# Performance work log

Hardware: AMD Instinct MI355X
Metric: run time of the kernel (lower is better)

Reference implementation:

```python
import jax, jax.numpy as jnp
import numpy as np

N_NODES = 100000
N_EDGES = 1000000
VOCAB = 128
EMB = 64
HID = 64
N_CLASSES = 2
N_GRAPHS = 2048


def setup_inputs() -> dict:
    key = jax.random.key(0)
    ks = jax.random.split(key, 12)
    x = jax.random.randint(ks[0], (N_NODES,), 0, VOCAB)
    edge_index = jax.random.randint(ks[1], (2, N_EDGES), 0, N_NODES)
    batch = jnp.sort(jax.random.randint(ks[2], (N_NODES,), 0, N_GRAPHS))

    def glorot(k, shape):
        fan = shape[0]
        return jax.random.normal(k, shape, dtype=jnp.float32) / np.sqrt(fan).astype(np.float32)

    emb = jax.random.normal(ks[3], (VOCAB, EMB), dtype=jnp.float32)
    W1_l = glorot(ks[4], (EMB, HID)); b1 = jnp.zeros((HID,), jnp.float32)
    W1_r = glorot(ks[5], (EMB, HID))
    W2_l = glorot(ks[6], (HID, HID)); b2 = jnp.zeros((HID,), jnp.float32)
    W2_r = glorot(ks[7], (HID, HID))
    W_out = glorot(ks[8], (HID, N_CLASSES)); b_out = jnp.zeros((N_CLASSES,), jnp.float32)
    return {"x": x, "edge_index": edge_index, "batch": batch, "emb": emb,
            "W1_l": W1_l, "b1": b1, "W1_r": W1_r,
            "W2_l": W2_l, "b2": b2, "W2_r": W2_r,
            "W_out": W_out, "b_out": b_out}


def _sage_conv(h, src, dst, Wl, bl, Wr):
    # PyG SAGEConv: out = lin_l(mean_{j in N(i)} h_j) + lin_r(h_i); lin_r has no bias
    msgs = h[src]                                                        # [E, D] gather
    agg = jax.ops.segment_sum(msgs, dst, num_segments=N_NODES)          # [N, D] scatter-add
    cnt = jax.ops.segment_sum(jnp.ones((src.shape[0], 1), h.dtype), dst,
                              num_segments=N_NODES)                      # [N, 1] degree
    mean = agg / jnp.maximum(cnt, 1.0)
    return mean @ Wl + bl + h @ Wr


def reference(x, edge_index, batch, emb, W1_l, b1, W1_r, W2_l, b2, W2_r, W_out, b_out):
    src, dst = edge_index[0], edge_index[1]
    h = emb[x]                                                           # [N, EMB]
    h = jax.nn.relu(_sage_conv(h, src, dst, W1_l, b1, W1_r))             # [N, HID]
    h = jax.nn.relu(_sage_conv(h, src, dst, W2_l, b2, W2_r))             # [N, HID]
    # global_mean_pool over graph ids
    gsum = jax.ops.segment_sum(h, batch, num_segments=N_GRAPHS)          # [G, HID]
    gcnt = jax.ops.segment_sum(jnp.ones((N_NODES, 1), h.dtype), batch,
                               num_segments=N_GRAPHS)
    pooled = gsum / jnp.maximum(gcnt, 1.0)
    return pooled @ W_out + b_out                                        # [G, C]
```

## Files before the change

kernel.cpp:

```cpp
#include <hip/hip_runtime.h>
#include <hip/hip_bf16.h>

#define N_NODES 100000
#define N_EDGES 1000000
#define EMB 64
#define HID 64
#define VOCAB 128
#define N_GRAPHS 2048

#define CBUCKET 256
#define NBK ((N_NODES + CBUCKET - 1) / CBUCKET)
#define CAP 4096
#define CHUNK 4096
#define SCAT_BLOCKS ((N_EDGES + CHUNK - 1) / CHUNK)
#define GB ((N_NODES + 255) / 256)
#define ZROW N_NODES

#define BCASTF(v, l) __int_as_float(__builtin_amdgcn_readlane(__float_as_int(v), (l)))

typedef __attribute__((ext_vector_type(8))) short short8;
typedef __attribute__((ext_vector_type(4))) float f32x4;
typedef __attribute__((ext_vector_type(2))) float f32x2;

__device__ __forceinline__ float bf2f(unsigned short u) {
    return __uint_as_float((unsigned)u << 16);
}
__device__ __forceinline__ float bf2f_lo(unsigned u) {
    return __uint_as_float(u << 16);
}
__device__ __forceinline__ float bf2f_hi(unsigned u) {
    return __uint_as_float(u & 0xffff0000u);
}
__device__ __forceinline__ unsigned short f2bf(float f) {
    return __bfloat16_as_ushort(__float2bfloat16(f));
}

__global__ __launch_bounds__(256) void scatter_kernel(
    const int* __restrict__ src, const int* __restrict__ dst,
    const int* __restrict__ x,
    int* __restrict__ cursor, unsigned* __restrict__ edge8,
    const int* __restrict__ batch, int* __restrict__ gstart,
    const float* __restrict__ emb, const float* __restrict__ W1l,
    const float* __restrict__ W1r,
    const float* __restrict__ W2l, const float* __restrict__ W2r,
    float* __restrict__ embW1l, float* __restrict__ embW1r,
    unsigned short* __restrict__ w2frag, unsigned char* __restrict__ p8z)
{
    __shared__ unsigned earr[CHUNK];
    __shared__ unsigned short karr[CHUNK];
    __shared__ int bcnt[NBK];
    __shared__ int bbase[NBK];
    int b = blockIdx.x;
    int t = threadIdx.x;

    if (b < SCAT_BLOCKS) {
        for (int i = t; i < NBK; i += 256) bcnt[i] = 0;
        __syncthreads();
        int e0 = b * CHUNK;
        int n = min(e0 + CHUNK, N_EDGES) - e0;
        for (int i = t; i < n; i += 256) {
            int d = dst[e0 + i];
            int s = src[e0 + i];
            int xv = x[s];
            int k = d >> 8;
            earr[i] = (unsigned)s | ((unsigned)xv << 17) | ((unsigned)(d & 255) << 24);
            karr[i] = (unsigned short)k;
            atomicAdd(&bcnt[k], 1);
        }
        __syncthreads();
        for (int i = t; i < NBK; i += 256) {
            int c = bcnt[i];
            bbase[i] = i * CAP + (c ? atomicAdd(&cursor[i], c) : 0);
            bcnt[i] = 0;
        }
        __syncthreads();
        for (int i = t; i < n; i += 256) {
            int k = karr[i];
            int off = atomicAdd(&bcnt[k], 1);
            edge8[bbase[k] + off] = earr[i];
        }
    } else if (b < SCAT_BLOCKS + GB) {
        int i = (b - SCAT_BLOCKS) * 256 + t;
        if (i >= N_NODES) return;
        int bg = batch[i];
        int bp = (i == 0) ? -1 : batch[i - 1];
        for (int g = bp + 1; g <= bg; ++g) gstart[g] = i;
        if (i == N_NODES - 1)
            for (int g = bg + 1; g <= N_GRAPHS; ++g) gstart[g] = N_NODES;
    } else {
        int vb = b - SCAT_BLOCKS - GB;
        if (vb == 0 && t < 16)
            ((unsigned*)(p8z + (size_t)N_NODES * 64))[t] = 0u;
        int wave = t >> 6, lane = t & 63;
        int v = vb * 4 + wave;
        if (v < VOCAB) {
            float er = emb[v * 64 + lane];
            float al = 0.f, ar = 0.f;
#pragma unroll 8
            for (int d = 0; d < 64; ++d) {
                float e = BCASTF(er, d);
                al += e * W1l[d * 64 + lane];
                ar += e * W1r[d * 64 + lane];
            }
            embW1l[v * 64 + lane] = al;
            embW1r[v * 64 + lane] = ar;
        }
        int g = vb * 256 + t;
        int j = g & 7, l = (g >> 3) & 63, h = (g >> 9) & 1, tt = g >> 10;
        int k = h * 32 + ((l >> 4) * 8) + j;
        int n = tt * 16 + (l & 15);
        float w = (n < 64) ? W2l[k * 64 + n] : W2r[k * 64 + (n - 64)];
        w2frag[g] = f2bf(w);
    }
}

__global__ __launch_bounds__(256) void csr_kernel(
    const unsigned* __restrict__ edge8, const int* __restrict__ cursor,
    int* __restrict__ row_start, int* __restrict__ deg, int* __restrict__ col,
    int* __restrict__ col16,
    const float* __restrict__ embW1l, const float* __restrict__ embW1r,
    unsigned short* __restrict__ w1frag)
{
    __shared__ int cnt[CBUCKET];
    __shared__ int scn[CBUCKET];
    __shared__ int exs[CBUCKET];
    int b = blockIdx.x;
    int t = threadIdx.x;

    for (int i = t * 4; i < CBUCKET * 16; i += 1024)
        *(int4*)&col16[b * CBUCKET * 16 + i] = (int4){ZROW, ZROW, ZROW, ZROW};

    if (b < 8) {
        int g0 = (b * 256 + t) * 8;
#pragma unroll
        for (int j = 0; j < 8; ++j) {
            int g = g0 + j;
            int fi = g >> 9;
            int kf = fi >> 2, nt = fi & 3;
            int l = (g >> 3) & 63, jj = g & 7;
            int kg = kf * 32 + ((l >> 4) << 3) + jj;
            int n = nt * 16 + (l & 15);
            float w = (kg < 128) ? embW1l[kg * 64 + n] : embW1r[(kg - 128) * 64 + n];
            w1frag[g] = f2bf(w);
        }
    }

    int lo = b * CAP, hi = lo + cursor[b];
    cnt[t] = 0;
    __syncthreads();
    for (int i = lo + t; i < hi; i += 256)
        atomicAdd(&cnt[edge8[i] >> 24], 1);
    __syncthreads();
    int v = cnt[t];
    scn[t] = v;
    __syncthreads();
    for (int off = 1; off < 256; off <<= 1) {
        int tmp = (t >= off) ? scn[t - off] : 0;
        __syncthreads();
        scn[t] += tmp;
        __syncthreads();
    }
    int excl = scn[t] - v;
    int node = b * CBUCKET + t;
    if (node < N_NODES) { row_start[node] = lo + excl; deg[node] = v; }
    cnt[t] = excl;
    exs[t] = excl;
    __syncthreads();
    for (int i = lo + t; i < hi; i += 256) {
        unsigned e = edge8[i];
        int ld = (int)(e >> 24);
        int slot = atomicAdd(&cnt[ld], 1);
        col[lo + slot] = (int)(e & 0xFFFFFF);
        int local = slot - exs[ld];
        if (local < 16)
            col16[(b * CBUCKET + ld) * 16 + local] = (int)(e & 0x1FFFF);
    }
}

__global__ __launch_bounds__(256) void sage1_kernel(
    const int* __restrict__ x, const int* __restrict__ deg,
    const unsigned* __restrict__ edge8, const int* __restrict__ cursor,
    const unsigned short* __restrict__ w1frag,
    const unsigned short* __restrict__ w2frag, const float* __restrict__ b1,
    unsigned char* __restrict__ p8, unsigned short* __restrict__ q16)
{
    __shared__ unsigned hist[128 * 32];
    __shared__ unsigned short msbuf[128 * 72];
    __shared__ int xl[128];
    __shared__ float invd[128];

    int blk = blockIdx.x, bucket = blk >> 1, half = blk & 1;
    int t = threadIdx.x;
    int nbase = bucket * CBUCKET + half * 128;

    for (int i = t * 4; i < 128 * 32; i += 1024)
        *(uint4*)&hist[i] = (uint4){0u, 0u, 0u, 0u};
    if (t < 128) {
        int node = nbase + t;
        int dv = (node < N_NODES) ? deg[node] : 0;
        invd[t] = 1.0f / fmaxf((float)dv, 1.0f);
        xl[t] = (node < N_NODES) ? x[node] : 0;
    }
    __syncthreads();

    int lo = bucket * CAP, ecnt = cursor[bucket];
    for (int i = t; i < ecnt; i += 256) {
        unsigned e = edge8[lo + i];
        int ld = (int)(e >> 24);
        if ((ld >> 7) == half) {
            int r = ld & 127;
            int xv = (int)((e >> 17) & 127);
            int wc = (xv >> 2) ^ ((r & 7) << 2);
            atomicAdd(&hist[r * 32 + wc], 1u << ((xv & 3) * 8));
        }
    }
    __syncthreads();

    int wave = t >> 6, lane = t & 63;
    int m = lane & 15;
    int qd = lane >> 4;
    int hswz = (m & 7) << 2;

#pragma unroll
    for (int rt = wave * 2; rt < wave * 2 + 2; ++rt) {
        short8 acnt[4], aself[4];
#pragma unroll
        for (int kf = 0; kf < 4; ++kf) {
            int w0 = (kf * 8 + qd * 2) ^ hswz;
            uint2 u = *(const uint2*)&hist[(rt * 16 + m) * 32 + w0];
            short8 f;
            f[0] = (short)f2bf((float)(u.x & 255));
            f[1] = (short)f2bf((float)((u.x >> 8) & 255));
            f[2] = (short)f2bf((float)((u.x >> 16) & 255));
            f[3] = (short)f2bf((float)(u.x >> 24));
            f[4] = (short)f2bf((float)(u.y & 255));
            f[5] = (short)f2bf((float)((u.y >> 8) & 255));
            f[6] = (short)f2bf((float)((u.y >> 16) & 255));
            f[7] = (short)f2bf((float)(u.y >> 24));
            acnt[kf] = f;
        }
        int xv = xl[rt * 16 + m];
#pragma unroll
        for (int kf = 0; kf < 4; ++kf) {
            int v = xv - kf * 32 - qd * 8;
            short8 f;
#pragma unroll
            for (int j = 0; j < 8; ++j)
                f[j] = (v == j) ? (short)0x3F80 : (short)0;
            aself[kf] = f;
        }
        float iv0 = invd[rt * 16 + qd * 4 + 0];
        float iv1 = invd[rt * 16 + qd * 4 + 1];
        float iv2 = invd[rt * 16 + qd * 4 + 2];
        float iv3 = invd[rt * 16 + qd * 4 + 3];

#pragma unroll
        for (int nt = 0; nt < 4; ++nt) {
            f32x4 accA = {0.f, 0.f, 0.f, 0.f};
            f32x4 accS = {0.f, 0.f, 0.f, 0.f};
#pragma unroll
            for (int kf = 0; kf < 4; ++kf) {
                short8 bA = *(const short8*)(w1frag + ((kf * 4 + nt) * 64 + lane) * 8);
                accA = __builtin_amdgcn_mfma_f32_16x16x32_bf16(acnt[kf], bA, accA, 0, 0, 0);
            }
#pragma unroll
            for (int kf = 0; kf < 4; ++kf) {
                short8 bS = *(const short8*)(w1frag + (((kf + 4) * 4 + nt) * 64 + lane) * 8);
                accS = __builtin_amdgcn_mfma_f32_16x16x32_bf16(aself[kf], bS, accS, 0, 0, 0);
            }
            int c = nt * 16 + m;
            float b1c = b1[c];
            int rb = rt * 16 + qd * 4;
            msbuf[(rb + 0) * 72 + c] = f2bf(fmaxf(accA[0] * iv0 + accS[0] + b1c, 0.f));
            msbuf[(rb + 1) * 72 + c] = f2bf(fmaxf(accA[1] * iv1 + accS[1] + b1c, 0.f));
            msbuf[(rb + 2) * 72 + c] = f2bf(fmaxf(accA[2] * iv2 + accS[2] + b1c, 0.f));
            msbuf[(rb + 3) * 72 + c] = f2bf(fmaxf(accA[3] * iv3 + accS[3] + b1c, 0.f));
        }
    }
    __syncthreads();

#pragma unroll
    for (int rt = wave * 2; rt < wave * 2 + 2; ++rt) {
        const unsigned short* arow = &msbuf[(rt * 16 + m) * 72 + qd * 8];
        short8 a0 = *(const short8*)(arow);
        short8 a1 = *(const short8*)(arow + 32);
        int rowb = nbase + rt * 16 + qd * 4;

#pragma unroll
        for (int tt = 0; tt < 8; ++tt) {
            short8 b0 = *(const short8*)(w2frag + tt * 1024 + lane * 8);
            short8 b1v = *(const short8*)(w2frag + tt * 1024 + 512 + lane * 8);
            f32x4 acc = {0.f, 0.f, 0.f, 0.f};
            acc = __builtin_amdgcn_mfma_f32_16x16x32_bf16(a0, b0, acc, 0, 0, 0);
            acc = __builtin_amdgcn_mfma_f32_16x16x32_bf16(a1, b1v, acc, 0, 0, 0);
            int o = tt * 16 + m;
            if (o < 64) {
                int pk01 = __builtin_amdgcn_cvt_pk_fp8_f32(acc[0], acc[1], 0, false);
                int pk23 = __builtin_amdgcn_cvt_pk_fp8_f32(acc[2], acc[3], 0, false);
                if (rowb + 0 < N_NODES) p8[(rowb + 0) * 64 + o] = (unsigned char)(pk01 & 0xff);
                if (rowb + 1 < N_NODES) p8[(rowb + 1) * 64 + o] = (unsigned char)((pk01 >> 8) & 0xff);
                if (rowb + 2 < N_NODES) p8[(rowb + 2) * 64 + o] = (unsigned char)(pk23 & 0xff);
                if (rowb + 3 < N_NODES) p8[(rowb + 3) * 64 + o] = (unsigned char)((pk23 >> 8) & 0xff);
            } else {
                int oc = o & 63;
#pragma unroll
                for (int i = 0; i < 4; ++i)
                    if (rowb + i < N_NODES)
                        q16[(rowb + i) * 64 + oc] = f2bf(acc[i]);
            }
        }
    }
}

#define S2_NPW 8
__global__ __launch_bounds__(256) void sage2_kernel(
    const unsigned char* __restrict__ p, const unsigned short* __restrict__ q,
    const int* __restrict__ row_start, const int* __restrict__ deg,
    const int* __restrict__ col, const int* __restrict__ col16,
    const float* __restrict__ b2,
    const float* __restrict__ Wout, const int* __restrict__ batch,
    float* __restrict__ gsum)
{
    int t = threadIdx.x;
    int wave = t >> 6, lane = t & 63;
    int base_node = (blockIdx.x * 4 + wave) * S2_NPW;
    int c = lane & 15;
    int g = lane >> 4;

    float4 b2v = ((const float4*)b2)[c];
    float4 w01 = ((const float4*)Wout)[c * 2];
    float4 w23 = ((const float4*)Wout)[c * 2 + 1];

    int dgs[S2_NPW];
#pragma unroll
    for (int n = 0; n < S2_NPW; ++n)
        dgs[n] = deg[base_node + n];

#define ACC(a, v) { f32x2 f01_ = __builtin_amdgcn_cvt_pk_f32_fp8((int)(v), false); \
                    f32x2 f23_ = __builtin_amdgcn_cvt_pk_f32_fp8((int)(v), true);  \
                    (a).x += f01_.x; (a).y += f01_.y; (a).z += f23_.x; (a).w += f23_.y; }

#pragma unroll
    for (int hb = 0; hb < 2; ++hb) {
        int nb = hb * 4;

        unsigned vc = (unsigned)((base_node + nb) * 64 + g * 4);
        unsigned i00, i01, i02, i03, i10, i11, i12, i13;
        unsigned i20, i21, i22, i23, i30, i31, i32, i33;
        asm volatile(
            "global_load_dword %0,  %16, %17\n\t"
            "global_load_dword %1,  %16, %17 offset:16\n\t"
            "global_load_dword %2,  %16, %17 offset:32\n\t"
            "global_load_dword %3,  %16, %17 offset:48\n\t"
            "global_load_dword %4,  %16, %17 offset:64\n\t"
            "global_load_dword %5,  %16, %17 offset:80\n\t"
            "global_load_dword %6,  %16, %17 offset:96\n\t"
            "global_load_dword %7,  %16, %17 offset:112\n\t"
            "global_load_dword %8,  %16, %17 offset:128\n\t"
            "global_load_dword %9,  %16, %17 offset:144\n\t"
            "global_load_dword %10, %16, %17 offset:160\n\t"
            "global_load_dword %11, %16, %17 offset:176\n\t"
            "global_load_dword %12, %16, %17 offset:192\n\t"
            "global_load_dword %13, %16, %17 offset:208\n\t"
            "global_load_dword %14, %16, %17 offset:224\n\t"
            "global_load_dword %15, %16, %17 offset:240\n\t"
            "s_waitcnt vmcnt(0)"
            : "=&v"(i00), "=&v"(i01), "=&v"(i02), "=&v"(i03),
              "=&v"(i10), "=&v"(i11), "=&v"(i12), "=&v"(i13),
              "=&v"(i20), "=&v"(i21), "=&v"(i22), "=&v"(i23),
              "=&v"(i30), "=&v"(i31), "=&v"(i32), "=&v"(i33)
            : "v"(vc), "s"(col16)
            : "memory");

        unsigned cc4 = (unsigned)(c << 2);
        unsigned o00 = (i00 << 6) + cc4, o01 = (i01 << 6) + cc4;
        unsigned o02 = (i02 << 6) + cc4, o03 = (i03 << 6) + cc4;
        unsigned o10 = (i10 << 6) + cc4, o11 = (i11 << 6) + cc4;
        unsigned o12 = (i12 << 6) + cc4, o13 = (i13 << 6) + cc4;
        unsigned o20 = (i20 << 6) + cc4, o21 = (i21 << 6) + cc4;
        unsigned o22 = (i22 << 6) + cc4, o23 = (i23 << 6) + cc4;
        unsigned o30 = (i30 << 6) + cc4, o31 = (i31 << 6) + cc4;
        unsigned o32 = (i32 << 6) + cc4, o33 = (i33 << 6) + cc4;
        unsigned vq = (unsigned)((base_node + nb) * 128 + c * 8);

        unsigned v00, v01, v02, v03, v10, v11, v12, v13;
        unsigned v20, v21, v22, v23, v30, v31, v32, v33;
        unsigned qa0, qb0, qa1, qb1, qa2, qb2, qa3, qb3;
        asm volatile(
            "global_load_dword %0,  %24, %41\n\t"
            "global_load_dword %1,  %25, %41\n\t"
            "global_load_dword %2,  %26, %41\n\t"
            "global_load_dword %3,  %27, %41\n\t"
            "global_load_dword %4,  %28, %41\n\t"
            "global_load_dword %5,  %29, %41\n\t"
            "global_load_dword %6,  %30, %41\n\t"
            "global_load_dword %7,  %31, %41\n\t"
            "global_load_dword %8,  %32, %41\n\t"
            "global_load_dword %9,  %33, %41\n\t"
            "global_load_dword %10, %34, %41\n\t"
            "global_load_dword %11, %35, %41\n\t"
            "global_load_dword %12, %36, %41\n\t"
            "global_load_dword %13, %37, %41\n\t"
            "global_load_dword %14, %38, %41\n\t"
            "global_load_dword %15, %39, %41\n\t"
            "global_load_dword %16, %40, %42\n\t"
            "global_load_dword %17, %40, %42 offset:4\n\t"
            "global_load_dword %18, %40, %42 offset:128\n\t"
            "global_load_dword %19, %40, %42 offset:132\n\t"
            "global_load_dword %20, %40, %42 offset:256\n\t"
            "global_load_dword %21, %40, %42 offset:260\n\t"
            "global_load_dword %22, %40, %42 offset:384\n\t"
            "global_load_dword %23, %40, %42 offset:388\n\t"
            "s_waitcnt vmcnt(0)"
            : "=&v"(v00), "=&v"(v01), "=&v"(v02), "=&v"(v03),
              "=&v"(v10), "=&v"(v11), "=&v"(v12), "=&v"(v13),
              "=&v"(v20), "=&v"(v21), "=&v"(v22), "=&v"(v23),
              "=&v"(v30), "=&v"(v31), "=&v"(v32), "=&v"(v33),
              "=&v"(qa0), "=&v"(qb0), "=&v"(qa1), "=&v"(qb1),
              "=&v"(qa2), "=&v"(qb2), "=&v"(qa3), "=&v"(qb3)
            : "v"(o00), "v"(o01), "v"(o02), "v"(o03),
              "v"(o10), "v"(o11), "v"(o12), "v"(o13),
              "v"(o20), "v"(o21), "v"(o22), "v"(o23),
              "v"(o30), "v"(o31), "v"(o32), "v"(o33),
              "v"(vq), "s"(p), "s"(q)
            : "memory");

#pragma unroll
        for (int pp = 0; pp < 2; ++pp) {
            int na = nb + pp * 2, nbd = nb + pp * 2 + 1;
            int dgA = dgs[na], dgB = dgs[nbd];

            float4 aA = {0.f,0.f,0.f,0.f}, aB = {0.f,0.f,0.f,0.f};
            if (pp == 0) {
                ACC(aA, v00) ACC(aA, v01) ACC(aA, v02) ACC(aA, v03)
                ACC(aB, v10) ACC(aB, v11) ACC(aB, v12) ACC(aB, v13)
            } else {
                ACC(aA, v20) ACC(aA, v21) ACC(aA, v22) ACC(aA, v23)
                ACC(aB, v30) ACC(aB, v31) ACC(aB, v32) ACC(aB, v33)
            }

            if (dgA > 16) {
                int rsA = row_start[base_node + na];
                for (int j = 16; j < dgA; j += 8) {
                    int r0 = j + g, r1 = j + 4 + g;
                    int i0 = (r0 < dgA) ? (col[rsA + r0] & 0x1FFFF) : ZROW;
                    int i1 = (r1 < dgA) ? (col[rsA + r1] & 0x1FFFF) : ZROW;
                    unsigned u0 = *(const unsigned*)(p + (size_t)i0 * 64 + c * 4);
                    unsigned u1 = *(const unsigned*)(p + (size_t)i1 * 64 + c * 4);
                    ACC(aA, u0) ACC(aA, u1)
                }
            }
            if (dgB > 16) {
                int rsB = row_start[base_node + nbd];
                for (int j = 16; j < dgB; j += 8) {
                    int r0 = j + g, r1 = j + 4 + g;
                    int i0 = (r0 < dgB) ? (col[rsB + r0] & 0x1FFFF) : ZROW;
                    int i1 = (r1 < dgB) ? (col[rsB + r1] & 0x1FFFF) : ZROW;
                    unsigned u0 = *(const unsigned*)(p + (size_t)i0 * 64 + c * 4);
                    unsigned u1 = *(const unsigned*)(p + (size_t)i1 * 64 + c * 4);
                    ACC(aB, u0) ACC(aB, u1)
                }
            }

            aA.x += __shfl_xor(aA.x, 16, 64); aA.y += __shfl_xor(aA.y, 16, 64);
            aA.z += __shfl_xor(aA.z, 16, 64); aA.w += __shfl_xor(aA.w, 16, 64);
            aB.x += __shfl_xor(aB.x, 16, 64); aB.y += __shfl_xor(aB.y, 16, 64);
            aB.z += __shfl_xor(aB.z, 16, 64); aB.w += __shfl_xor(aB.w, 16, 64);
            aA.x += __shfl_xor(aA.x, 32, 64); aA.y += __shfl_xor(aA.y, 32, 64);
            aA.z += __shfl_xor(aA.z, 32, 64); aA.w += __shfl_xor(aA.w, 32, 64);
            aB.x += __shfl_xor(aB.x, 32, 64); aB.y += __shfl_xor(aB.y, 32, 64);
            aB.z += __shfl_xor(aB.z, 32, 64); aB.w += __shfl_xor(aB.w, 32, 64);

#pragma unroll
            for (int e = 0; e < 2; ++e) {
                int node = base_node + nb + pp * 2 + e;
                int dg = (e == 0) ? dgA : dgB;
                float4 a = (e == 0) ? aA : aB;
                int li = pp * 2 + e;
                unsigned qlo = (li == 0) ? qa0 : (li == 1) ? qa1 : (li == 2) ? qa2 : qa3;
                unsigned qhi = (li == 0) ? qb0 : (li == 1) ? qb1 : (li == 2) ? qb2 : qb3;
                float inv = 1.0f / fmaxf((float)dg, 1.0f);
                float h0 = fmaxf(a.x * inv + b2v.x + bf2f_lo(qlo), 0.f);
                float h1 = fmaxf(a.y * inv + b2v.y + bf2f_hi(qlo), 0.f);
                float h2 = fmaxf(a.z * inv + b2v.z + bf2f_lo(qhi), 0.f);
                float h3 = fmaxf(a.w * inv + b2v.w + bf2f_hi(qhi), 0.f);

                float p0 = h0 * w01.x + h1 * w01.z + h2 * w23.x + h3 * w23.z;
                float p1 = h0 * w01.y + h1 * w01.w + h2 * w23.y + h3 * w23.w;
                if (g != 0) { p0 = 0.f; p1 = 0.f; }
                p0 += __shfl_down(p0, 8, 64);  p1 += __shfl_down(p1, 8, 64);
                p0 += __shfl_down(p0, 4, 64);  p1 += __shfl_down(p1, 4, 64);
                p0 += __shfl_down(p0, 2, 64);  p1 += __shfl_down(p1, 2, 64);
                p0 += __shfl_down(p0, 1, 64);  p1 += __shfl_down(p1, 1, 64);
                if (lane == 0) {
                    int grp = batch[node];
                    atomicAdd(&gsum[grp * 2 + 0], p0);
                    atomicAdd(&gsum[grp * 2 + 1], p1);
                }
            }
        }
    }
#undef ACC
}

__global__ __launch_bounds__(256) void finalize_kernel(
    const float* __restrict__ gsum, const int* __restrict__ gstart,
    const float* __restrict__ bout, float* __restrict__ out)
{
    int g = blockIdx.x * 256 + threadIdx.x;
    if (g >= N_GRAPHS) return;
    int cnt = gstart[g + 1] - gstart[g];
    float inv = 1.0f / fmaxf((float)cnt, 1.0f);
    out[g * 2 + 0] = gsum[g * 2 + 0] * inv + bout[0];
    out[g * 2 + 1] = gsum[g * 2 + 1] * inv + bout[1];
}

extern "C" void kernel_launch(void* const* d_in, const int* in_sizes, int n_in,
                              void* d_out, int out_size, void* d_ws, size_t ws_size,
                              hipStream_t stream) {
    const int*   x    = (const int*)  d_in[0];
    const int*   ei   = (const int*)  d_in[1];
    const int*   batch= (const int*)  d_in[2];
    const float* emb  = (const float*)d_in[3];
    const float* W1l  = (const float*)d_in[4];
    const float* b1   = (const float*)d_in[5];
    const float* W1r  = (const float*)d_in[6];
    const float* W2l  = (const float*)d_in[7];
    const float* b2   = (const float*)d_in[8];
    const float* W2r  = (const float*)d_in[9];
    const float* Wout = (const float*)d_in[10];
    const float* bout = (const float*)d_in[11];
    float* out = (float*)d_out;

    const int* src = ei;
    const int* dst = ei + N_EDGES;

    char* ws = (char*)d_ws;
    size_t off = 0;
    unsigned char*  p8     = (unsigned char*) (ws + off); off += (size_t)N_NODES * 64 + 64;
    unsigned short* q16    = (unsigned short*)(ws + off); off += (size_t)N_NODES * 64 * 2;
    unsigned short* w2frag = (unsigned short*)(ws + off); off += (size_t)8192 * 2;
    unsigned short* w1frag = (unsigned short*)(ws + off); off += (size_t)16384 * 2;
    float*    embW1l = (float*)   (ws + off); off += (size_t)VOCAB * 64 * 4;
    float*    embW1r = (float*)   (ws + off); off += (size_t)VOCAB * 64 * 4;
    int*      rowst  = (int*)     (ws + off); off += (size_t)N_NODES * 4;
    int*      deg    = (int*)     (ws + off); off += (size_t)N_NODES * 4;
    int*      col    = (int*)     (ws + off); off += (size_t)(NBK * CAP + 256) * 4;
    int*      col16  = (int*)     (ws + off); off += (size_t)NBK * CBUCKET * 16 * 4;
    unsigned* edge8  = (unsigned*)(ws + off); off += (size_t)NBK * CAP * 4;
    int*      gstart = (int*)     (ws + off); off += (size_t)(N_GRAPHS + 1) * 4;
    int*      cursor = (int*)     (ws + off); off += (size_t)NBK * 4;
    float*    gsum   = (float*)   (ws + off); off += (size_t)N_GRAPHS * 2 * 4;

    hipMemsetAsync(cursor, 0, (size_t)NBK * 4 + (size_t)N_GRAPHS * 2 * 4, stream);

    scatter_kernel<<<SCAT_BLOCKS + GB + 32, 256, 0, stream>>>(
        src, dst, x, cursor, edge8,
        batch, gstart, emb, W1l, W1r, W2l, W2r, embW1l, embW1r, w2frag, p8);
    csr_kernel<<<NBK, 256, 0, stream>>>(edge8, cursor, rowst, deg, col, col16,
                                        embW1l, embW1r, w1frag);
    sage1_kernel<<<NBK * 2, 256, 0, stream>>>(
        x, deg, edge8, cursor, w1frag, w2frag, b1, p8, q16);
    sage2_kernel<<<N_NODES / (4 * S2_NPW), 256, 0, stream>>>(
        p8, q16, rowst, deg, col, col16, b2, Wout, batch, gsum);
    finalize_kernel<<<(N_GRAPHS + 255) / 256, 256, 0, stream>>>(gsum, gstart, bout, out);
}
```

Baseline: 196.1 us.

## Replace bucketed CSR build with fixed 32-slot per-node adjacency plus overflow list

Drops the two-pass bucket scatter and the csr_kernel. Edges are now written directly into a padded 32-slot-per-node array, using a global per-destination atomic counter, and edges beyond 32 go to a global overflow list. The embedding-times-W1 results are written straight into the bf16 MFMA fragment layout, which removes one kernel launch and the intermediate buffers. The cost is about a million global atomics on random addresses. High-degree nodes also make a linear scan over the whole overflow list in sage2, and the overflow path truncates edges if it exceeds its fixed capacity.

```diff
diff --git a/kernel.cpp b/kernel.cpp
--- a/kernel.cpp
+++ b/kernel.cpp
@@ -8,13 +8,12 @@
 #define VOCAB 128
 #define N_GRAPHS 2048
 
-#define CBUCKET 256
-#define NBK ((N_NODES + CBUCKET - 1) / CBUCKET)
-#define CAP 4096
-#define CHUNK 4096
-#define SCAT_BLOCKS ((N_EDGES + CHUNK - 1) / CHUNK)
+#define S_BLOCKS 1024
 #define GB ((N_NODES + 255) / 256)
-#define ZROW N_NODES
+#define NB1 ((N_NODES + 127) / 128)
+#define NPAD 100128
+#define OVF_CAP 65536
+#define ZROW 0x1FFFF
 
 #define BCASTF(v, l) __int_as_float(__builtin_amdgcn_readlane(__float_as_int(v), (l)))
 
@@ -38,49 +37,34 @@
 __global__ __launch_bounds__(256) void scatter_kernel(
     const int* __restrict__ src, const int* __restrict__ dst,
     const int* __restrict__ x,
-    int* __restrict__ cursor, unsigned* __restrict__ edge8,
+    int* __restrict__ dcnt, int* __restrict__ col32,
+    int2* __restrict__ ovf, int* __restrict__ ovf_cnt,
     const int* __restrict__ batch, int* __restrict__ gstart,
     const float* __restrict__ emb, const float* __restrict__ W1l,
     const float* __restrict__ W1r,
     const float* __restrict__ W2l, const float* __restrict__ W2r,
-    float* __restrict__ embW1l, float* __restrict__ embW1r,
-    unsigned short* __restrict__ w2frag, unsigned char* __restrict__ p8z)
+    unsigned short* __restrict__ w1frag, unsigned short* __restrict__ w2frag,
+    unsigned char* __restrict__ p8z)
 {
-    __shared__ unsigned earr[CHUNK];
-    __shared__ unsigned short karr[CHUNK];
-    __shared__ int bcnt[NBK];
-    __shared__ int bbase[NBK];
     int b = blockIdx.x;
     int t = threadIdx.x;
 
-    if (b < SCAT_BLOCKS) {
-        for (int i = t; i < NBK; i += 256) bcnt[i] = 0;
-        __syncthreads();
-        int e0 = b * CHUNK;
-        int n = min(e0 + CHUNK, N_EDGES) - e0;
-        for (int i = t; i < n; i += 256) {
-            int d = dst[e0 + i];
-            int s = src[e0 + i];
+    if (b < S_BLOCKS) {
+        for (int i = b * 256 + t; i < N_EDGES; i += S_BLOCKS * 256) {
+            int d = dst[i];
+            int s = src[i];
             int xv = x[s];
-            int k = d >> 8;
-            earr[i] = (unsigned)s | ((unsigned)xv << 17) | ((unsigned)(d & 255) << 24);
-            karr[i] = (unsigned short)k;
-            atomicAdd(&bcnt[k], 1);
-        }
-        __syncthreads();
-        for (int i = t; i < NBK; i += 256) {
-            int c = bcnt[i];
-            bbase[i] = i * CAP + (c ? atomicAdd(&cursor[i], c) : 0);
-            bcnt[i] = 0;
-        }
-        __syncthreads();
-        for (int i = t; i < n; i += 256) {
-            int k = karr[i];
-            int off = atomicAdd(&bcnt[k], 1);
-            edge8[bbase[k] + off] = earr[i];
-        }
-    } else if (b < SCAT_BLOCKS + GB) {
-        int i = (b - SCAT_BLOCKS) * 256 + t;
+            int pay = s | (xv << 17);
+            int slot = atomicAdd(&dcnt[d], 1);
+            if (slot < 32) {
+                col32[(size_t)d * 32 + slot] = pay;
+            } else {
+                int w = atomicAdd(ovf_cnt, 1);
+                if (w < OVF_CAP) ovf[w] = make_int2(d, pay);
+            }
+        }
+    } else if (b < S_BLOCKS + GB) {
+        int i = (b - S_BLOCKS) * 256 + t;
         if (i >= N_NODES) return;
         int bg = batch[i];
         int bp = (i == 0) ? -1 : batch[i - 1];
@@ -88,12 +72,13 @@
         if (i == N_NODES - 1)
             for (int g = bg + 1; g <= N_GRAPHS; ++g) gstart[g] = N_NODES;
     } else {
-        int vb = b - SCAT_BLOCKS - GB;
+        int vb = b - S_BLOCKS - GB;
         if (vb == 0 && t < 16)
-            ((unsigned*)(p8z + (size_t)N_NODES * 64))[t] = 0u;
+            ((unsigned*)(p8z + (size_t)ZROW * 64))[t] = 0u;
+
         int wave = t >> 6, lane = t & 63;
         int v = vb * 4 + wave;
-        if (v < VOCAB) {
+        {
             float er = emb[v * 64 + lane];
             float al = 0.f, ar = 0.f;
 #pragma unroll 8
@@ -102,8 +87,13 @@
                 al += e * W1l[d * 64 + lane];
                 ar += e * W1r[d * 64 + lane];
             }
-            embW1l[v * 64 + lane] = al;
-            embW1r[v * 64 + lane] = ar;
+            int reml = (v >> 3) & 3, jj = v & 7;
+            int ll = (reml << 4) | (lane & 15);
+            int nt = lane >> 4;
+            int gl = ((((v >> 5)) * 4 + nt) * 64 + ll) * 8 + jj;
+            int gr = ((((v >> 5) + 4) * 4 + nt) * 64 + ll) * 8 + jj;
+            w1frag[gl] = f2bf(al);
+            w1frag[gr] = f2bf(ar);
         }
         int g = vb * 256 + t;
         int j = g & 7, l = (g >> 3) & 63, h = (g >> 9) & 1, tt = g >> 10;
@@ -114,72 +104,10 @@
     }
 }
 
-__global__ __launch_bounds__(256) void csr_kernel(
-    const unsigned* __restrict__ edge8, const int* __restrict__ cursor,
-    int* __restrict__ row_start, int* __restrict__ deg, int* __restrict__ col,
-    int* __restrict__ col16,
-    const float* __restrict__ embW1l, const float* __restrict__ embW1r,
-    unsigned short* __restrict__ w1frag)
-{
-    __shared__ int cnt[CBUCKET];
-    __shared__ int scn[CBUCKET];
-    __shared__ int exs[CBUCKET];
-    int b = blockIdx.x;
-    int t = threadIdx.x;
-
-    for (int i = t * 4; i < CBUCKET * 16; i += 1024)
-        *(int4*)&col16[b * CBUCKET * 16 + i] = (int4){ZROW, ZROW, ZROW, ZROW};
-
-    if (b < 8) {
-        int g0 = (b * 256 + t) * 8;
-#pragma unroll
-        for (int j = 0; j < 8; ++j) {
-            int g = g0 + j;
-            int fi = g >> 9;
-            int kf = fi >> 2, nt = fi & 3;
-            int l = (g >> 3) & 63, jj = g & 7;
-            int kg = kf * 32 + ((l >> 4) << 3) + jj;
-            int n = nt * 16 + (l & 15);
-            float w = (kg < 128) ? embW1l[kg * 64 + n] : embW1r[(kg - 128) * 64 + n];
-            w1frag[g] = f2bf(w);
-        }
-    }
-
-    int lo = b * CAP, hi = lo + cursor[b];
-    cnt[t] = 0;
-    __syncthreads();
-    for (int i = lo + t; i < hi; i += 256)
-        atomicAdd(&cnt[edge8[i] >> 24], 1);
-    __syncthreads();
-    int v = cnt[t];
-    scn[t] = v;
-    __syncthreads();
-    for (int off = 1; off < 256; off <<= 1) {
-        int tmp = (t >= off) ? scn[t - off] : 0;
-        __syncthreads();
-        scn[t] += tmp;
-        __syncthreads();
-    }
-    int excl = scn[t] - v;
-    int node = b * CBUCKET + t;
-    if (node < N_NODES) { row_start[node] = lo + excl; deg[node] = v; }
-    cnt[t] = excl;
-    exs[t] = excl;
-    __syncthreads();
-    for (int i = lo + t; i < hi; i += 256) {
-        unsigned e = edge8[i];
-        int ld = (int)(e >> 24);
-        int slot = atomicAdd(&cnt[ld], 1);
-        col[lo + slot] = (int)(e & 0xFFFFFF);
-        int local = slot - exs[ld];
-        if (local < 16)
-            col16[(b * CBUCKET + ld) * 16 + local] = (int)(e & 0x1FFFF);
-    }
-}
-
 __global__ __launch_bounds__(256) void sage1_kernel(
     const int* __restrict__ x, const int* __restrict__ deg,
-    const unsigned* __restrict__ edge8, const int* __restrict__ cursor,
+    const int* __restrict__ col32,
+    const int2* __restrict__ ovf, const int* __restrict__ ovf_cnt,
     const unsigned short* __restrict__ w1frag,
     const unsigned short* __restrict__ w2frag, const float* __restrict__ b1,
     unsigned char* __restrict__ p8, unsigned short* __restrict__ q16)
@@ -187,29 +115,39 @@
     __shared__ unsigned hist[128 * 32];
     __shared__ unsigned short msbuf[128 * 72];
     __shared__ int xl[128];
+    __shared__ int degl[128];
     __shared__ float invd[128];
 
-    int blk = blockIdx.x, bucket = blk >> 1, half = blk & 1;
+    int blk = blockIdx.x;
     int t = threadIdx.x;
-    int nbase = bucket * CBUCKET + half * 128;
+    int nbase = blk * 128;
 
     for (int i = t * 4; i < 128 * 32; i += 1024)
         *(uint4*)&hist[i] = (uint4){0u, 0u, 0u, 0u};
     if (t < 128) {
         int node = nbase + t;
-        int dv = (node < N_NODES) ? deg[node] : 0;
+        int dv = deg[node];
+        degl[t] = dv;
         invd[t] = 1.0f / fmaxf((float)dv, 1.0f);
         xl[t] = (node < N_NODES) ? x[node] : 0;
     }
     __syncthreads();
 
-    int lo = bucket * CAP, ecnt = cursor[bucket];
-    for (int i = t; i < ecnt; i += 256) {
-        unsigned e = edge8[lo + i];
-        int ld = (int)(e >> 24);
-        if ((ld >> 7) == half) {
-            int r = ld & 127;
+    for (int i = t; i < 128 * 32; i += 256) {
+        int r = i >> 5, j = i & 31;
+        if (j < degl[r]) {
+            unsigned e = (unsigned)col32[(size_t)(nbase + r) * 32 + j];
             int xv = (int)((e >> 17) & 127);
+            int wc = (xv >> 2) ^ ((r & 7) << 2);
+            atomicAdd(&hist[r * 32 + wc], 1u << ((xv & 3) * 8));
+        }
+    }
+    int ovn = *ovf_cnt; if (ovn > OVF_CAP) ovn = OVF_CAP;
+    for (int k = t; k < ovn; k += 256) {
+        int2 e = ovf[k];
+        int r = e.x - nbase;
+        if (r >= 0 && r < 128) {
+            int xv = (e.y >> 17) & 127;
             int wc = (xv >> 2) ^ ((r & 7) << 2);
             atomicAdd(&hist[r * 32 + wc], 1u << ((xv & 3) * 8));
         }
@@ -315,8 +253,8 @@
 #define S2_NPW 8
 __global__ __launch_bounds__(256) void sage2_kernel(
     const unsigned char* __restrict__ p, const unsigned short* __restrict__ q,
-    const int* __restrict__ row_start, const int* __restrict__ deg,
-    const int* __restrict__ col, const int* __restrict__ col16,
+    const int* __restrict__ deg, const int* __restrict__ col32,
+    const int2* __restrict__ ovf, const int* __restrict__ ovf_cnt,
     const float* __restrict__ b2,
     const float* __restrict__ Wout, const int* __restrict__ batch,
     float* __restrict__ gsum)
@@ -344,7 +282,7 @@
     for (int hb = 0; hb < 2; ++hb) {
         int nb = hb * 4;
 
-        unsigned vc = (unsigned)((base_node + nb) * 64 + g * 4);
+        unsigned vc = (unsigned)((base_node + nb) * 128 + g * 4);
         unsigned i00, i01, i02, i03, i10, i11, i12, i13;
         unsigned i20, i21, i22, i23, i30, i31, i32, i33;
         asm volatile(
@@ -352,35 +290,38 @@
             "global_load_dword %1,  %16, %17 offset:16\n\t"
             "global_load_dword %2,  %16, %17 offset:32\n\t"
             "global_load_dword %3,  %16, %17 offset:48\n\t"
-            "global_load_dword %4,  %16, %17 offset:64\n\t"
-            "global_load_dword %5,  %16, %17 offset:80\n\t"
-            "global_load_dword %6,  %16, %17 offset:96\n\t"
-            "global_load_dword %7,  %16, %17 offset:112\n\t"
-            "global_load_dword %8,  %16, %17 offset:128\n\t"
-            "global_load_dword %9,  %16, %17 offset:144\n\t"
-            "global_load_dword %10, %16, %17 offset:160\n\t"
-            "global_load_dword %11, %16, %17 offset:176\n\t"
-            "global_load_dword %12, %16, %17 offset:192\n\t"
-            "global_load_dword %13, %16, %17 offset:208\n\t"
-            "global_load_dword %14, %16, %17 offset:224\n\t"
-            "global_load_dword %15, %16, %17 offset:240\n\t"
+            "global_load_dword %4,  %16, %17 offset:128\n\t"
+            "global_load_dword %5,  %16, %17 offset:144\n\t"
+            "global_load_dword %6,  %16, %17 offset:160\n\t"
+            "global_load_dword %7,  %16, %17 offset:176\n\t"
+            "global_load_dword %8,  %16, %17 offset:256\n\t"
+            "global_load_dword %9,  %16, %17 offset:272\n\t"
+            "global_load_dword %10, %16, %17 offset:288\n\t"
+            "global_load_dword %11, %16, %17 offset:304\n\t"
+            "global_load_dword %12, %16, %17 offset:384\n\t"
+            "global_load_dword %13, %16, %17 offset:400\n\t"
+            "global_load_dword %14, %16, %17 offset:416\n\t"
+            "global_load_dword %15, %16, %17 offset:432\n\t"
             "s_waitcnt vmcnt(0)"
             : "=&v"(i00), "=&v"(i01), "=&v"(i02), "=&v"(i03),
               "=&v"(i10), "=&v"(i11), "=&v"(i12), "=&v"(i13),
               "=&v"(i20), "=&v"(i21), "=&v"(i22), "=&v"(i23),
               "=&v"(i30), "=&v"(i31), "=&v"(i32), "=&v"(i33)
-            : "v"(vc), "s"(col16)
+            : "v"(vc), "s"(col32)
             : "memory");
 
         unsigned cc4 = (unsigned)(c << 2);
-        unsigned o00 = (i00 << 6) + cc4, o01 = (i01 << 6) + cc4;
-        unsigned o02 = (i02 << 6) + cc4, o03 = (i03 << 6) + cc4;
-        unsigned o10 = (i10 << 6) + cc4, o11 = (i11 << 6) + cc4;
-        unsigned o12 = (i12 << 6) + cc4, o13 = (i13 << 6) + cc4;
-        unsigned o20 = (i20 << 6) + cc4, o21 = (i21 << 6) + cc4;
-        unsigned o22 = (i22 << 6) + cc4, o23 = (i23 << 6) + cc4;
-        unsigned o30 = (i30 << 6) + cc4, o31 = (i31 << 6) + cc4;
-        unsigned o32 = (i32 << 6) + cc4, o33 = (i33 << 6) + cc4;
+        int d0 = dgs[nb + 0], d1 = dgs[nb + 1], d2 = dgs[nb + 2], d3 = dgs[nb + 3];
+#define SEL(i_, dg_, k_) ((((k_) * 4 + g) < (dg_)) ? ((i_) & 0x1FFFFu) : (unsigned)ZROW)
+        unsigned o00 = (SEL(i00, d0, 0) << 6) + cc4, o01 = (SEL(i01, d0, 1) << 6) + cc4;
+        unsigned o02 = (SEL(i02, d0, 2) << 6) + cc4, o03 = (SEL(i03, d0, 3) << 6) + cc4;
+        unsigned o10 = (SEL(i10, d1, 0) << 6) + cc4, o11 = (SEL(i11, d1, 1) << 6) + cc4;
+        unsigned o12 = (SEL(i12, d1, 2) << 6) + cc4, o13 = (SEL(i13, d1, 3) << 6) + cc4;
+        unsigned o20 = (SEL(i20, d2, 0) << 6) + cc4, o21 = (SEL(i21, d2, 1) << 6) + cc4;
+        unsigned o22 = (SEL(i22, d2, 2) << 6) + cc4, o23 = (SEL(i23, d2, 3) << 6) + cc4;
+        unsigned o30 = (SEL(i30, d3, 0) << 6) + cc4, o31 = (SEL(i31, d3, 1) << 6) + cc4;
+        unsigned o32 = (SEL(i32, d3, 2) << 6) + cc4, o33 = (SEL(i33, d3, 3) << 6) + cc4;
+#undef SEL
         unsigned vq = (unsigned)((base_node + nb) * 128 + c * 8);
 
         unsigned v00, v01, v02, v03, v10, v11, v12, v13;
@@ -429,6 +370,7 @@
         for (int pp = 0; pp < 2; ++pp) {
             int na = nb + pp * 2, nbd = nb + pp * 2 + 1;
             int dgA = dgs[na], dgB = dgs[nbd];
+            int nodeA = base_node + na, nodeB = base_node + nbd;
 
             float4 aA = {0.f,0.f,0.f,0.f}, aB = {0.f,0.f,0.f,0.f};
             if (pp == 0) {
@@ -440,25 +382,45 @@
             }
 
             if (dgA > 16) {
-                int rsA = row_start[base_node + na];
-                for (int j = 16; j < dgA; j += 8) {
+                for (int j = 16; j < 32 && j < dgA; j += 8) {
                     int r0 = j + g, r1 = j + 4 + g;
-                    int i0 = (r0 < dgA) ? (col[rsA + r0] & 0x1FFFF) : ZROW;
-                    int i1 = (r1 < dgA) ? (col[rsA + r1] & 0x1FFFF) : ZROW;
-                    unsigned u0 = *(const unsigned*)(p + (size_t)i0 * 64 + c * 4);
-                    unsigned u1 = *(const unsigned*)(p + (size_t)i1 * 64 + c * 4);
+                    unsigned i0 = (r0 < dgA) ? ((unsigned)col32[(size_t)nodeA * 32 + r0] & 0x1FFFFu) : (unsigned)ZROW;
+                    unsigned i1 = (r1 < dgA) ? ((unsigned)col32[(size_t)nodeA * 32 + r1] & 0x1FFFFu) : (unsigned)ZROW;
+                    unsigned u0 = *(const unsigned*)(p + ((size_t)i0 << 6) + c * 4);
+                    unsigned u1 = *(const unsigned*)(p + ((size_t)i1 << 6) + c * 4);
                     ACC(aA, u0) ACC(aA, u1)
                 }
+                if (dgA > 32) {
+                    int ovn = *ovf_cnt; if (ovn > OVF_CAP) ovn = OVF_CAP;
+                    for (int k = 0; k < ovn; ++k) {
+                        int2 e = ovf[k];
+                        if (e.x == nodeA) {
+                            unsigned i_ = (unsigned)e.y & 0x1FFFFu;
+                            unsigned u = *(const unsigned*)(p + ((size_t)i_ << 6) + c * 4);
+                            if (g == 0) ACC(aA, u)
+                        }
+                    }
+                }
             }
             if (dgB > 16) {
-                int rsB = row_start[base_node + nbd];
-                for (int j = 16; j < dgB; j += 8) {
+                for (int j = 16; j < 32 && j < dgB; j += 8) {
                     int r0 = j + g, r1 = j + 4 + g;
-                    int i0 = (r0 < dgB) ? (col[rsB + r0] & 0x1FFFF) : ZROW;
-                    int i1 = (r1 < dgB) ? (col[rsB + r1] & 0x1FFFF) : ZROW;
-                    unsigned u0 = *(const unsigned*)(p + (size_t)i0 * 64 + c * 4);
-                    unsigned u1 = *(const unsigned*)(p + (size_t)i1 * 64 + c * 4);
+                    unsigned i0 = (r0 < dgB) ? ((unsigned)col32[(size_t)nodeB * 32 + r0] & 0x1FFFFu) : (unsigned)ZROW;
+                    unsigned i1 = (r1 < dgB) ? ((unsigned)col32[(size_t)nodeB * 32 + r1] & 0x1FFFFu) : (unsigned)ZROW;
+                    unsigned u0 = *(const unsigned*)(p + ((size_t)i0 << 6) + c * 4);
+                    unsigned u1 = *(const unsigned*)(p + ((size_t)i1 << 6) + c * 4);
                     ACC(aB, u0) ACC(aB, u1)
+                }
+                if (dgB > 32) {
+                    int ovn = *ovf_cnt; if (ovn > OVF_CAP) ovn = OVF_CAP;
+                    for (int k = 0; k < ovn; ++k) {
+                        int2 e = ovf[k];
+                        if (e.x == nodeB) {
+                            unsigned i_ = (unsigned)e.y & 0x1FFFFu;
+                            unsigned u = *(const unsigned*)(p + ((size_t)i_ << 6) + c * 4);
+                            if (g == 0) ACC(aB, u)
+                        }
+                    }
                 }
             }
 
@@ -537,31 +499,25 @@
 
     char* ws = (char*)d_ws;
     size_t off = 0;
-    unsigned char*  p8     = (unsigned char*) (ws + off); off += (size_t)N_NODES * 64 + 64;
+    unsigned char*  p8     = (unsigned char*) (ws + off); off += (size_t)(ZROW + 1) * 64;
     unsigned short* q16    = (unsigned short*)(ws + off); off += (size_t)N_NODES * 64 * 2;
     unsigned short* w2frag = (unsigned short*)(ws + off); off += (size_t)8192 * 2;
     unsigned short* w1frag = (unsigned short*)(ws + off); off += (size_t)16384 * 2;
-    float*    embW1l = (float*)   (ws + off); off += (size_t)VOCAB * 64 * 4;
-    float*    embW1r = (float*)   (ws + off); off += (size_t)VOCAB * 64 * 4;
-    int*      rowst  = (int*)     (ws + off); off += (size_t)N_NODES * 4;
-    int*      deg    = (int*)     (ws + off); off += (size_t)N_NODES * 4;
-    int*      col    = (int*)     (ws + off); off += (size_t)(NBK * CAP + 256) * 4;
-    int*      col16  = (int*)     (ws + off); off += (size_t)NBK * CBUCKET * 16 * 4;
-    unsigned* edge8  = (unsigned*)(ws + off); off += (size_t)NBK * CAP * 4;
-    int*      gstart = (int*)     (ws + off); off += (size_t)(N_GRAPHS + 1) * 4;
-    int*      cursor = (int*)     (ws + off); off += (size_t)NBK * 4;
+    int*      col32  = (int*)     (ws + off); off += (size_t)NPAD * 32 * 4;
+    int2*     ovf    = (int2*)    (ws + off); off += (size_t)OVF_CAP * 8;
+    int*      gstart = (int*)     (ws + off); off += (size_t)(N_GRAPHS + 2) * 4;
+    int*      dcnt   = (int*)     (ws + off); off += (size_t)NPAD * 4;
+    int*      ovfcnt = (int*)     (ws + off); off += (size_t)4;
     float*    gsum   = (float*)   (ws + off); off += (size_t)N_GRAPHS * 2 * 4;
 
-    hipMemsetAsync(cursor, 0, (size_t)NBK * 4 + (size_t)N_GRAPHS * 2 * 4, stream);
-
-    scatter_kernel<<<SCAT_BLOCKS + GB + 32, 256, 0, stream>>>(
-        src, dst, x, cursor, edge8,
-        batch, gstart, emb, W1l, W1r, W2l, W2r, embW1l, embW1r, w2frag, p8);
-    csr_kernel<<<NBK, 256, 0, stream>>>(edge8, cursor, rowst, deg, col, col16,
-                                        embW1l, embW1r, w1frag);
-    sage1_kernel<<<NBK * 2, 256, 0, stream>>>(
-        x, deg, edge8, cursor, w1frag, w2frag, b1, p8, q16);
+    hipMemsetAsync(dcnt, 0, (size_t)NPAD * 4 + 4 + (size_t)N_GRAPHS * 2 * 4, stream);
+
+    scatter_kernel<<<S_BLOCKS + GB + 32, 256, 0, stream>>>(
+        src, dst, x, dcnt, col32, ovf, ovfcnt,
+        batch, gstart, emb, W1l, W1r, W2l, W2r, w1frag, w2frag, p8);
+    sage1_kernel<<<NB1, 256, 0, stream>>>(
+        x, dcnt, col32, ovf, ovfcnt, w1frag, w2frag, b1, p8, q16);
     sage2_kernel<<<N_NODES / (4 * S2_NPW), 256, 0, stream>>>(
-        p8, q16, rowst, deg, col, col16, b2, Wout, batch, gsum);
+        p8, q16, dcnt, col32, ovf, ovfcnt, b2, Wout, batch, gsum);
     finalize_kernel<<<(N_GRAPHS + 255) / 256, 256, 0, stream>>>(gsum, gstart, bout, out);
 }
```

After: 219.1 us. +11.8%, slower.
